# Kernel optimization log

Measured on AMD Instinct MI355X. Metric: run time of the kernel, lower is better.

Reference implementation:

```python
import jax, jax.numpy as jnp
import numpy as np
import math

N_FREQS = 32
MARGIN = 0.1
CHOUT = 270
POS_DIM = 2 * N_FREQS ** 2  # 2048


def fourier_emb(positions):
    # positions: [..., 2] in [0, 1]
    width = 1.0 + 2.0 * MARGIN
    p = (positions + MARGIN) / width
    f = jnp.arange(N_FREQS, dtype=p.dtype)
    two_pi = 2.0 * math.pi
    # phase[..., i, j] = 2*pi*(x*i + y*j)  -> flatten to [..., F*F]
    phase = two_pi * (p[..., 0][..., None, None] * f[:, None]
                      + p[..., 1][..., None, None] * f[None, :])
    phase = phase.reshape(*phase.shape[:-2], N_FREQS * N_FREQS)
    return jnp.concatenate([jnp.sin(phase), jnp.cos(phase)], axis=-1)  # [..., 2F^2]


def setup_inputs() -> dict:
    key = jax.random.key(0)
    k1, k2, k3 = jax.random.split(key, 3)
    B, C, T = 32, 273, 3000
    brain_data = jax.random.normal(k1, (B, C, T), dtype=jnp.float32)
    channel_layout = jax.random.uniform(k2, (B, C, 2), dtype=jnp.float32)
    heads = jax.random.normal(k3, (CHOUT, POS_DIM), dtype=jnp.float32) / POS_DIM ** 0.5
    return {"brain_data": brain_data, "channel_layout": channel_layout, "heads": heads}


def reference(brain_data, channel_layout, heads):
    # Eval mode: all channels valid, no dropout mask, zero score offset.
    emb = fourier_emb(channel_layout)                      # [B, C, D]
    scores = jnp.einsum('bcd,od->boc', emb, heads)         # [B, O, C]
    weights = jax.nn.softmax(scores, axis=-1)              # softmax over channels
    out = jnp.einsum('bct,boc->bot', brain_data, weights)  # [B, O, T]
    return out
```

## Files before the change

### kernel.cpp

```cpp
#include <hip/hip_runtime.h>
#include <hip/hip_bf16.h>
#include <hip/hip_fp16.h>

#define NB 32
#define NC 273
#define NT 3000
#define NO 270
#define ND 2048
#define CP 288

typedef _Float16 f16x8 __attribute__((ext_vector_type(8)));
typedef float f32x4 __attribute__((ext_vector_type(4)));

#define S_OFF 55296000UL
#define W_OFF 64730880UL
#define H_OFF 69707520UL

__global__ void heads_cvt_kernel(const float* __restrict__ heads,
                                 _Float16* __restrict__ hh) {
  const size_t idx = ((size_t)blockIdx.x * 256 + threadIdx.x) * 8;
  const float4 a = *reinterpret_cast<const float4*>(heads + idx);
  const float4 c = *reinterpret_cast<const float4*>(heads + idx + 4);
  f16x8 v;
  v[0] = (_Float16)a.x; v[1] = (_Float16)a.y; v[2] = (_Float16)a.z; v[3] = (_Float16)a.w;
  v[4] = (_Float16)c.x; v[5] = (_Float16)c.y; v[6] = (_Float16)c.z; v[7] = (_Float16)c.w;
  *reinterpret_cast<f16x8*>(hh + idx) = v;
}

__global__ void scores_kernel(const _Float16* __restrict__ hh,
                              const float* __restrict__ layout,
                              float* __restrict__ scores) {
  __shared__ _Float16 As[64][72];
  __shared__ _Float16 Bs[64][72];
  const int gid = blockIdx.x;
  const int tid = threadIdx.x;
  const int b = gid / 25;
  const int rem = gid % 25;
  const int o0 = (rem / 5) * 64;
  const int c0 = (rem % 5) * 64;
  const int lane = tid & 63, w = tid >> 6;
  const int wm = (w >> 1) * 32, wn = (w & 1) * 32;
  const int ln = lane & 15, quad = lane >> 4;
  const int sr = tid >> 2;
  const int sk = (tid & 3) * 16;

  const int ch = c0 + sr;
  float px = 0.f, py = 0.f;
  if (ch < NC) {
    const float inv = 1.0f / 1.2f;
    const float* lp = layout + ((size_t)b * NC + ch) * 2;
    px = (lp[0] + 0.1f) * inv;
    py = (lp[1] + 0.1f) * inv;
  }

  f32x4 acc[2][2] = {};

  for (int k0 = 0; k0 < ND; k0 += 64) {
    {
      const int o = o0 + sr;
      uint4 u0 = {0, 0, 0, 0}, u1 = {0, 0, 0, 0};
      if (o < NO) {
        const uint4* p = reinterpret_cast<const uint4*>(hh + (size_t)o * ND + k0 + sk);
        u0 = p[0]; u1 = p[1];
      }
      *reinterpret_cast<uint4*>(&As[sr][sk]) = u0;
      *reinterpret_cast<uint4*>(&As[sr][sk + 8]) = u1;
    }
    {
      const int kg = k0 + sk;
      const int dd = kg & 1023;
      const float base = px * (float)(dd >> 5) + py * (float)(dd & 31)
                       + ((kg < 1024) ? 0.0f : 0.25f);
      f16x8 h0, h1;
#pragma unroll
      for (int s = 0; s < 8; ++s) {
        float ph = base + py * (float)s;
        ph -= floorf(ph);
        h0[s] = (_Float16)__builtin_amdgcn_sinf(ph);
      }
#pragma unroll
      for (int s = 0; s < 8; ++s) {
        float ph = base + py * (float)(s + 8);
        ph -= floorf(ph);
        h1[s] = (_Float16)__builtin_amdgcn_sinf(ph);
      }
      *reinterpret_cast<f16x8*>(&Bs[sr][sk]) = h0;
      *reinterpret_cast<f16x8*>(&Bs[sr][sk + 8]) = h1;
    }
    __syncthreads();
#pragma unroll
    for (int ks = 0; ks < 64; ks += 32) {
      const int kf = ks + quad * 8;
      const f16x8 a0 = *reinterpret_cast<const f16x8*>(&As[wm + ln][kf]);
      const f16x8 a1 = *reinterpret_cast<const f16x8*>(&As[wm + 16 + ln][kf]);
      const f16x8 b0 = *reinterpret_cast<const f16x8*>(&Bs[wn + ln][kf]);
      const f16x8 b1 = *reinterpret_cast<const f16x8*>(&Bs[wn + 16 + ln][kf]);
      acc[0][0] = __builtin_amdgcn_mfma_f32_16x16x32_f16(a0, b0, acc[0][0], 0, 0, 0);
      acc[0][1] = __builtin_amdgcn_mfma_f32_16x16x32_f16(a0, b1, acc[0][1], 0, 0, 0);
      acc[1][0] = __builtin_amdgcn_mfma_f32_16x16x32_f16(a1, b0, acc[1][0], 0, 0, 0);
      acc[1][1] = __builtin_amdgcn_mfma_f32_16x16x32_f16(a1, b1, acc[1][1], 0, 0, 0);
    }
    __syncthreads();
  }

  float* sB = scores + (size_t)b * NO * NC;
#pragma unroll
  for (int i = 0; i < 2; ++i) {
    const int ob = o0 + wm + 16 * i + quad * 4;
#pragma unroll
    for (int j = 0; j < 2; ++j) {
      const int cc = c0 + wn + 16 * j + ln;
      if (cc >= NC) continue;
#pragma unroll
      for (int r = 0; r < 4; ++r) {
        const int o = ob + r;
        if (o < NO) sB[(size_t)o * NC + cc] = acc[i][j][r];
      }
    }
  }
}

__global__ void softmax_kernel(const float* __restrict__ sc,
                               _Float16* __restrict__ wq) {
  const int row = blockIdx.x * 4 + (threadIdx.x >> 6);
  const int lane = threadIdx.x & 63;
  const float* p = sc + (size_t)row * NC;
  _Float16* q = wq + (size_t)row * CP;
  float v[5];
  float m = -3.0e38f;
#pragma unroll
  for (int k = 0; k < 5; ++k) {
    const int c = lane + k * 64;
    v[k] = (c < NC) ? p[c] : -3.0e38f;
    m = fmaxf(m, v[k]);
  }
#pragma unroll
  for (int off = 32; off > 0; off >>= 1) m = fmaxf(m, __shfl_xor(m, off));
  float s = 0.f;
#pragma unroll
  for (int k = 0; k < 5; ++k) {
    v[k] = expf(v[k] - m);
    s += v[k];
  }
#pragma unroll
  for (int off = 32; off > 0; off >>= 1) s += __shfl_xor(s, off);
  const float r = 1.0f / s;
#pragma unroll
  for (int k = 0; k < 5; ++k) {
    const int c = lane + k * 64;
    if (c < NC) q[c] = (_Float16)(v[k] * r);
    else if (c < CP) q[c] = (_Float16)0.f;
  }
}

#define TS 64

__global__ void out_kernel(const _Float16* __restrict__ wq,
                           const float* __restrict__ brain,
                           float* __restrict__ out) {
  __shared__ _Float16 As[64][296];
  __shared__ _Float16 Bs[TS][296];
  const int b = blockIdx.y;
  const int t0 = blockIdx.x * TS;
  const int tid = threadIdx.x;
  const int lane = tid & 63, w = tid >> 6;
  const int wm = (w >> 1) * 32, wn = (w & 1) * 32;
  const int ln = lane & 15, quad = lane >> 4;

  {
    const int cw = tid >> 4;
    const int tl = (tid & 15) * 4;
#pragma unroll 6
    for (int p = 0; p < 18; ++p) {
      const int c = p * 16 + cw;
      float4 v = {0.f, 0.f, 0.f, 0.f};
      if (c < NC) {
        const int t = t0 + tl;
        const float* src = brain + ((size_t)b * NC + c) * NT + t;
        if (t + 3 < NT) {
          v = *reinterpret_cast<const float4*>(src);
        } else {
          if (t + 0 < NT) v.x = src[0];
          if (t + 1 < NT) v.y = src[1];
          if (t + 2 < NT) v.z = src[2];
        }
      }
      Bs[tl + 0][c] = (_Float16)v.x;
      Bs[tl + 1][c] = (_Float16)v.y;
      Bs[tl + 2][c] = (_Float16)v.z;
      Bs[tl + 3][c] = (_Float16)v.w;
    }
  }

  const _Float16* Wb = wq + (size_t)b * NO * CP;
  float* oB = out + (size_t)b * NO * NT;

  for (int ot = 0; ot < 5; ++ot) {
    const int o0 = ot * 64;
    {
      const int row = tid >> 2;
      const int o = o0 + row;
#pragma unroll
      for (int k = 0; k < 9; ++k) {
        const int col = (tid & 3) * 8 + k * 32;
        uint4 u = {0, 0, 0, 0};
        if (o < NO) u = *reinterpret_cast<const uint4*>(Wb + (size_t)o * CP + col);
        *reinterpret_cast<uint4*>(&As[row][col]) = u;
      }
    }
    __syncthreads();

    f32x4 acc[2][2] = {};
#pragma unroll
    for (int s = 0; s < 9; ++s) {
      const int kf = s * 32 + quad * 8;
      const f16x8 a0 = *reinterpret_cast<const f16x8*>(&As[wm + ln][kf]);
      const f16x8 a1 = *reinterpret_cast<const f16x8*>(&As[wm + 16 + ln][kf]);
      const f16x8 b0 = *reinterpret_cast<const f16x8*>(&Bs[wn + ln][kf]);
      const f16x8 b1 = *reinterpret_cast<const f16x8*>(&Bs[wn + 16 + ln][kf]);
      acc[0][0] = __builtin_amdgcn_mfma_f32_16x16x32_f16(a0, b0, acc[0][0], 0, 0, 0);
      acc[0][1] = __builtin_amdgcn_mfma_f32_16x16x32_f16(a0, b1, acc[0][1], 0, 0, 0);
      acc[1][0] = __builtin_amdgcn_mfma_f32_16x16x32_f16(a1, b0, acc[1][0], 0, 0, 0);
      acc[1][1] = __builtin_amdgcn_mfma_f32_16x16x32_f16(a1, b1, acc[1][1], 0, 0, 0);
    }

#pragma unroll
    for (int i = 0; i < 2; ++i) {
      const int ob = o0 + wm + 16 * i + quad * 4;
#pragma unroll
      for (int j = 0; j < 2; ++j) {
        const int t = t0 + wn + 16 * j + ln;
        if (t >= NT) continue;
#pragma unroll
        for (int r = 0; r < 4; ++r) {
          const int o = ob + r;
          if (o < NO) oB[(size_t)o * NT + t] = acc[i][j][r];
        }
      }
    }
    __syncthreads();
  }
}

extern "C" void kernel_launch(void* const* d_in, const int* in_sizes, int n_in,
                              void* d_out, int out_size, void* d_ws, size_t ws_size,
                              hipStream_t stream) {
  const float* brain = (const float*)d_in[0];
  const float* layout = (const float*)d_in[1];
  const float* heads = (const float*)d_in[2];
  for (int i = 0; i < n_in; ++i) {
    if (in_sizes[i] == NB * NC * NT) brain = (const float*)d_in[i];
    else if (in_sizes[i] == NB * NC * 2) layout = (const float*)d_in[i];
    else if (in_sizes[i] == NO * ND) heads = (const float*)d_in[i];
  }
  float* out = (float*)d_out;

  float* scores = (float*)((char*)d_ws + S_OFF);
  _Float16* wq = (_Float16*)((char*)d_ws + W_OFF);
  _Float16* hh = (_Float16*)((char*)d_ws + H_OFF);

  heads_cvt_kernel<<<NO, 256, 0, stream>>>(heads, hh);
  scores_kernel<<<800, 256, 0, stream>>>(hh, layout, scores);
  softmax_kernel<<<(NB * NO) / 4, 256, 0, stream>>>(scores, wq);
  out_kernel<<<dim3(47, NB), 256, 0, stream>>>(wq, brain, out);
}
```

Measured before the change: 290.3 us.

## Transpose brain tile via fp32 LDS staging and load weights directly from global

The brain tile load now stages fp32 values through a padded shared tile and converts them to packed fp16 with 16-byte LDS writes. This replaces the scattered 2-byte transposed stores that caused bank conflicts. The weight operand is now read straight from global/L2 into registers, with row indices clamped, which drops the As shared buffer and the per-o-tile barriers. The cost is two syncs per channel chunk and uncoalesced 16-byte global reads of the weights that rely on cache hits.

```diff
diff --git a/kernel.cpp b/kernel.cpp
--- a/kernel.cpp
+++ b/kernel.cpp
@@ -15,6 +15,13 @@
 #define S_OFF 55296000UL
 #define W_OFF 64730880UL
 #define H_OFF 69707520UL
+
+__device__ __forceinline__ unsigned short f2h_bits(float f) {
+  _Float16 h = (_Float16)f;
+  unsigned short u;
+  __builtin_memcpy(&u, &h, 2);
+  return u;
+}
 
 __global__ void heads_cvt_kernel(const float* __restrict__ heads,
                                  _Float16* __restrict__ hh) {
@@ -155,69 +162,80 @@
 
 #define TS 64
 
-__global__ void out_kernel(const _Float16* __restrict__ wq,
-                           const float* __restrict__ brain,
-                           float* __restrict__ out) {
-  __shared__ _Float16 As[64][296];
+__global__ __launch_bounds__(256) void out_kernel(
+    const _Float16* __restrict__ wq,
+    const float* __restrict__ brain,
+    float* __restrict__ out) {
   __shared__ _Float16 Bs[TS][296];
+  __shared__ float tile[32][68];
   const int b = blockIdx.y;
   const int t0 = blockIdx.x * TS;
   const int tid = threadIdx.x;
   const int lane = tid & 63, w = tid >> 6;
-  const int wm = (w >> 1) * 32, wn = (w & 1) * 32;
+  const int om = (w >> 1) * 32, tn = (w & 1) * 32;
   const int ln = lane & 15, quad = lane >> 4;
 
-  {
-    const int cw = tid >> 4;
-    const int tl = (tid & 15) * 4;
-#pragma unroll 6
-    for (int p = 0; p < 18; ++p) {
-      const int c = p * 16 + cw;
-      float4 v = {0.f, 0.f, 0.f, 0.f};
-      if (c < NC) {
-        const int t = t0 + tl;
-        const float* src = brain + ((size_t)b * NC + c) * NT + t;
-        if (t + 3 < NT) {
-          v = *reinterpret_cast<const float4*>(src);
-        } else {
-          if (t + 0 < NT) v.x = src[0];
-          if (t + 1 < NT) v.y = src[1];
-          if (t + 2 < NT) v.z = src[2];
-        }
-      }
-      Bs[tl + 0][c] = (_Float16)v.x;
-      Bs[tl + 1][c] = (_Float16)v.y;
-      Bs[tl + 2][c] = (_Float16)v.z;
-      Bs[tl + 3][c] = (_Float16)v.w;
-    }
+  const int cl = tid >> 3;
+  const int tq = (tid & 7) * 4;
+  const int tt = tid & 63;
+  const int cg = tid >> 6;
+  for (int p = 0; p < 9; ++p) {
+    const int c = p * 32 + cl;
+    float4 v0 = {0.f, 0.f, 0.f, 0.f}, v1 = v0;
+    if (c < NC) {
+      const float* src = brain + ((size_t)b * NC + c) * NT + t0 + tq;
+      const int tb = t0 + tq;
+      if (tb + 35 < NT) {
+        v0 = *reinterpret_cast<const float4*>(src);
+        v1 = *reinterpret_cast<const float4*>(src + 32);
+      } else {
+        if (tb + 0 < NT) v0.x = src[0];
+        if (tb + 1 < NT) v0.y = src[1];
+        if (tb + 2 < NT) v0.z = src[2];
+        if (tb + 3 < NT) v0.w = src[3];
+        if (tb + 32 < NT) v1.x = src[32];
+        if (tb + 33 < NT) v1.y = src[33];
+        if (tb + 34 < NT) v1.z = src[34];
+        if (tb + 35 < NT) v1.w = src[35];
+      }
+    }
+    *reinterpret_cast<float4*>(&tile[cl][tq]) = v0;
+    *reinterpret_cast<float4*>(&tile[cl][tq + 32]) = v1;
+    __syncthreads();
+    {
+      unsigned short h[8];
+#pragma unroll
+      for (int s = 0; s < 8; ++s) h[s] = f2h_bits(tile[cg * 8 + s][tt]);
+      uint4 u;
+      u.x = (unsigned)h[0] | ((unsigned)h[1] << 16);
+      u.y = (unsigned)h[2] | ((unsigned)h[3] << 16);
+      u.z = (unsigned)h[4] | ((unsigned)h[5] << 16);
+      u.w = (unsigned)h[6] | ((unsigned)h[7] << 16);
+      *reinterpret_cast<uint4*>(&Bs[tt][p * 32 + cg * 8]) = u;
+    }
+    __syncthreads();
   }
 
   const _Float16* Wb = wq + (size_t)b * NO * CP;
   float* oB = out + (size_t)b * NO * NT;
+  const int tA = tn + ln;
+  const int tB = tn + 16 + ln;
 
   for (int ot = 0; ot < 5; ++ot) {
     const int o0 = ot * 64;
-    {
-      const int row = tid >> 2;
-      const int o = o0 + row;
-#pragma unroll
-      for (int k = 0; k < 9; ++k) {
-        const int col = (tid & 3) * 8 + k * 32;
-        uint4 u = {0, 0, 0, 0};
-        if (o < NO) u = *reinterpret_cast<const uint4*>(Wb + (size_t)o * CP + col);
-        *reinterpret_cast<uint4*>(&As[row][col]) = u;
-      }
-    }
-    __syncthreads();
+    int ra = o0 + om + ln;      if (ra > NO - 1) ra = NO - 1;
+    int rb = o0 + om + 16 + ln; if (rb > NO - 1) rb = NO - 1;
+    const _Float16* pA0 = Wb + (size_t)ra * CP + quad * 8;
+    const _Float16* pA1 = Wb + (size_t)rb * CP + quad * 8;
 
     f32x4 acc[2][2] = {};
 #pragma unroll
     for (int s = 0; s < 9; ++s) {
-      const int kf = s * 32 + quad * 8;
-      const f16x8 a0 = *reinterpret_cast<const f16x8*>(&As[wm + ln][kf]);
-      const f16x8 a1 = *reinterpret_cast<const f16x8*>(&As[wm + 16 + ln][kf]);
-      const f16x8 b0 = *reinterpret_cast<const f16x8*>(&Bs[wn + ln][kf]);
-      const f16x8 b1 = *reinterpret_cast<const f16x8*>(&Bs[wn + 16 + ln][kf]);
+      const int kf = s * 32;
+      const f16x8 a0 = *reinterpret_cast<const f16x8*>(pA0 + kf);
+      const f16x8 a1 = *reinterpret_cast<const f16x8*>(pA1 + kf);
+      const f16x8 b0 = *reinterpret_cast<const f16x8*>(&Bs[tA][kf + quad * 8]);
+      const f16x8 b1 = *reinterpret_cast<const f16x8*>(&Bs[tB][kf + quad * 8]);
       acc[0][0] = __builtin_amdgcn_mfma_f32_16x16x32_f16(a0, b0, acc[0][0], 0, 0, 0);
       acc[0][1] = __builtin_amdgcn_mfma_f32_16x16x32_f16(a0, b1, acc[0][1], 0, 0, 0);
       acc[1][0] = __builtin_amdgcn_mfma_f32_16x16x32_f16(a1, b0, acc[1][0], 0, 0, 0);
@@ -226,10 +244,10 @@
 
 #pragma unroll
     for (int i = 0; i < 2; ++i) {
-      const int ob = o0 + wm + 16 * i + quad * 4;
+      const int ob = o0 + om + 16 * i + quad * 4;
 #pragma unroll
       for (int j = 0; j < 2; ++j) {
-        const int t = t0 + wn + 16 * j + ln;
+        const int t = t0 + tn + 16 * j + ln;
         if (t >= NT) continue;
 #pragma unroll
         for (int r = 0; r < 4; ++r) {
@@ -238,7 +256,6 @@
         }
       }
     }
-    __syncthreads();
   }
 }
 
```

Result: faster. 282.3 us (-2.8%).
